# Performance work log

Measured on AMD Instinct MI355X. Metric: run time of the kernel, lower is better.

The kernel has to match this reference:

```python
import jax, jax.numpy as jnp
import numpy as np
import math

EPS_PHI = 1e-4
EPS_DEN = 1e-6

B, H, N, D = 4, 16, 4096, 64
M = 128  # num random features


def _phi(x, omega, is_query):
    # x: [B,H,N,D], omega: [M,D] -> [B,H,N,M]
    proj = jnp.einsum('bhnd,md->bhnm', x, omega)
    log_phi = proj - 0.5 * jnp.sum(x * x, axis=-1, keepdims=True)
    if is_query:
        log_phi = log_phi - jnp.max(log_phi, axis=-1, keepdims=True)
    else:
        log_phi = log_phi - jnp.max(log_phi)
    return jnp.exp(log_phi) / math.sqrt(omega.shape[0]) + EPS_PHI


def setup_inputs() -> dict:
    key = jax.random.key(0)
    kq, kk, kv, ko = jax.random.split(key, 4)
    return {
        'q': jax.random.normal(kq, (B, H, N, D), dtype=jnp.float32),
        'k': jax.random.normal(kk, (B, H, N, D), dtype=jnp.float32),
        'v': jax.random.normal(kv, (B, H, N, D), dtype=jnp.float32),
        'omega': jax.random.normal(ko, (M, D), dtype=jnp.float32),
    }


def reference(q, k, v, omega):
    scale = q.shape[-1] ** (-0.25)
    phi_q = _phi(q * scale, omega, is_query=True).astype(jnp.float32)
    phi_k = _phi(k * scale, omega, is_query=False).astype(jnp.float32)
    vf = v.astype(jnp.float32)

    b, h, n, m = phi_q.shape
    d = vf.shape[-1]
    # time-major for scan: [N,B,H,*]
    pq_t = jnp.moveaxis(phi_q, 2, 0)
    pk_t = jnp.moveaxis(phi_k, 2, 0)
    v_t = jnp.moveaxis(vf, 2, 0)

    S0 = jnp.zeros((b, h, m, d), jnp.float32)
    z0 = jnp.zeros((b, h, m), jnp.float32)

    def step(carry, inp):
        S, z = carry
        pq_i, pk_i, v_i = inp  # [B,H,M], [B,H,M], [B,H,D]
        S = S + jnp.einsum('bhm,bhd->bhmd', pk_i, v_i)
        z = z + pk_i
        num = jnp.einsum('bhm,bhmd->bhd', pq_i, S)
        den = jnp.sum(pq_i * z, axis=-1, keepdims=True) + EPS_DEN
        return (S, z), num / den

    _, out_t = jax.lax.scan(step, (S0, z0), (pq_t, pk_t, v_t))
    out = jnp.moveaxis(out_t, 0, 2)  # [B,H,N,D]
    return out.astype(q.dtype)
```

## Files before the change

kernel.cpp:

```cpp
#include <hip/hip_runtime.h>
#include <math.h>

#define Bq 4
#define Hq 16
#define Nq 4096
#define Dq 64
#define Mq 128
#define Cq 32
#define Lq 128
#define EPS_PHI 1e-4f
#define EPS_DEN 1e-6f
#define SCALE 0.35355339059327373f
#define INVSQRT_M 0.08838834764831845f
#define STATE_STRIDE 8320

#define KSTR 136

#define PERM(m) (((m) & 15) * 8 + ((m) >> 4))

typedef __attribute__((ext_vector_type(8))) short bf16x8;
typedef __attribute__((ext_vector_type(4))) short s16x4;
typedef __attribute__((ext_vector_type(4))) float f32x4;

static __device__ inline f32x4 mfma16(bf16x8 a, bf16x8 b, f32x4 c) {
    return __builtin_amdgcn_mfma_f32_16x16x32_bf16(a, b, c, 0, 0, 0);
}

static __device__ inline unsigned short f2bf(float f) {
    unsigned u = __builtin_bit_cast(unsigned, f);
    u += 0x7FFF + ((u >> 16) & 1);
    return (unsigned short)(u >> 16);
}

static __device__ inline bf16x8 gfrag(const float* p, float scale) {
    float4 a = *(const float4*)p;
    float4 b = *(const float4*)(p + 4);
    union { bf16x8 v; unsigned short s[8]; } u;
    u.s[0] = f2bf(a.x * scale); u.s[1] = f2bf(a.y * scale);
    u.s[2] = f2bf(a.z * scale); u.s[3] = f2bf(a.w * scale);
    u.s[4] = f2bf(b.x * scale); u.s[5] = f2bf(b.y * scale);
    u.s[6] = f2bf(b.z * scale); u.s[7] = f2bf(b.w * scale);
    return u.v;
}

static __device__ inline bf16x8 gfrag_h(const float* p, float* hs) {
    float4 a = *(const float4*)p;
    float4 b = *(const float4*)(p + 4);
    float x0 = a.x * SCALE, x1 = a.y * SCALE, x2 = a.z * SCALE, x3 = a.w * SCALE;
    float x4 = b.x * SCALE, x5 = b.y * SCALE, x6 = b.z * SCALE, x7 = b.w * SCALE;
    *hs += x0 * x0 + x1 * x1 + x2 * x2 + x3 * x3
         + x4 * x4 + x5 * x5 + x6 * x6 + x7 * x7;
    union { bf16x8 v; unsigned short s[8]; } u;
    u.s[0] = f2bf(x0); u.s[1] = f2bf(x1); u.s[2] = f2bf(x2); u.s[3] = f2bf(x3);
    u.s[4] = f2bf(x4); u.s[5] = f2bf(x5); u.s[6] = f2bf(x6); u.s[7] = f2bf(x7);
    return u.v;
}

static __device__ inline bf16x8 ones_frag() {
    union { bf16x8 v; unsigned short s[8]; } u;
    #pragma unroll
    for (int i = 0; i < 8; ++i) u.s[i] = 0x3F80;
    return u.v;
}

__global__ __launch_bounds__(256) void vconv_kernel(
    const float* __restrict__ vin, unsigned short* __restrict__ vT,
    float* __restrict__ csumV) {
    __shared__ __align__(16) unsigned short vt_lds[64 * KSTR];
    __shared__ float csum[4][64];
    const int t = threadIdx.x;
    const int bx = blockIdx.x;
    const int bh = bx >> 5;
    const int l0 = (bx & 31) * Lq;
    const float* vb = vin + ((size_t)bh * Nq + l0) * 64;
    const int d = t & 63, g = t >> 6;

    float s = 0.f;
    #pragma unroll
    for (int rep = 0; rep < 32; ++rep) {
        int l = rep * 4 + g;
        float x = vb[(size_t)l * 64 + d];
        s += x;
        vt_lds[d * KSTR + l] = f2bf(x);
    }
    csum[g][d] = s;
    __syncthreads();
    if (t < 64)
        csumV[(size_t)bx * 64 + t] = csum[0][t] + csum[1][t] + csum[2][t] + csum[3][t];
    unsigned short* vTb = vT + (size_t)bh * 64 * Nq + l0;
    #pragma unroll
    for (int rep = 0; rep < 4; ++rep) {
        int idx = rep * 256 + t;
        int dd = idx >> 4, seg = idx & 15;
        *(bf16x8*)&vTb[(size_t)dd * Nq + seg * 8] =
            *(const bf16x8*)&vt_lds[dd * KSTR + seg * 8];
    }
}

__global__ __launch_bounds__(256) void oconv_kernel(
    const float* __restrict__ omega, unsigned short* __restrict__ omb) {
    const int t = threadIdx.x;
    #pragma unroll
    for (int rep = 0; rep < 4; ++rep) {
        int g8 = rep * 256 + t;
        const float* p = omega + (size_t)g8 * 8;
        float4 a = *(const float4*)p;
        float4 b = *(const float4*)(p + 4);
        union { bf16x8 v; unsigned short s[8]; } u;
        u.s[0] = f2bf(a.x); u.s[1] = f2bf(a.y); u.s[2] = f2bf(a.z); u.s[3] = f2bf(a.w);
        u.s[4] = f2bf(b.x); u.s[5] = f2bf(b.y); u.s[6] = f2bf(b.z); u.s[7] = f2bf(b.w);
        *(bf16x8*)&omb[(size_t)g8 * 8] = u.v;
    }
}

__global__ __launch_bounds__(512, 4) void chunkstate_kernel(
    const float* __restrict__ kin, const unsigned short* __restrict__ omb,
    const unsigned short* __restrict__ vT,
    float* __restrict__ partial, float* __restrict__ Sbuf) {
    __shared__ __align__(16) unsigned short PKt[128 * KSTR];
    __shared__ float wred[8];
    const int t = threadIdx.x, w = t >> 6, lane = t & 63;
    const int c16 = lane & 15, qd = lane >> 4;
    const int bx = blockIdx.x;
    const int bh = bx >> 5;
    const int l0 = (bx & 31) * Lq;
    const size_t rowbase = (size_t)bh * Nq + l0;
    const float* kb = kin + rowbase * 64;

    f32x4 acc[8];
    float ssum = 0.f;
    #pragma unroll
    for (int nt = 0; nt < 8; ++nt) acc[nt] = (f32x4){0.f, 0.f, 0.f, 0.f};
    #pragma unroll
    for (int kt = 0; kt < 2; ++kt) {
        bf16x8 a = gfrag_h(kb + (size_t)(16 * w + c16) * 64 + kt * 32 + qd * 8, &ssum);
        #pragma unroll
        for (int nt = 0; nt < 8; ++nt) {
            bf16x8 b = *(const bf16x8*)&omb[(size_t)(16 * nt + c16) * 64 + kt * 32 + qd * 8];
            acc[nt] = mfma16(a, b, acc[nt]);
        }
    }
    ssum += __shfl_xor(ssum, 16);
    ssum += __shfl_xor(ssum, 32);
    const float h_red = 0.5f * ssum;
    const int row0 = 16 * w + 4 * qd;
    float h4[4];
    #pragma unroll
    for (int r = 0; r < 4; ++r) h4[r] = __shfl(h_red, 4 * qd + r);

    float lmax = -1e30f;
    #pragma unroll
    for (int r = 0; r < 4; ++r) {
        #pragma unroll
        for (int nt = 0; nt < 8; ++nt) lmax = fmaxf(lmax, acc[nt][r] - h4[r]);
    }
    #pragma unroll
    for (int o = 1; o <= 32; o <<= 1) lmax = fmaxf(lmax, __shfl_xor(lmax, o));
    if (lane == 0) wred[w] = lmax;
    __syncthreads();
    float mc = wred[0];
    #pragma unroll
    for (int i = 1; i < 8; ++i) mc = fmaxf(mc, wred[i]);
    if (t == 0) partial[bx] = mc;

    #pragma unroll
    for (int nt = 0; nt < 8; ++nt) {
        union { s16x4 v; unsigned short s[4]; } u;
        #pragma unroll
        for (int r = 0; r < 4; ++r) {
            float pk = __expf(acc[nt][r] - h4[r] - mc) * INVSQRT_M;
            u.s[r] = f2bf(pk);
        }
        *(s16x4*)&PKt[(16 * nt + c16) * KSTR + row0] = u.v;
    }
    __syncthreads();

    const unsigned short* vTb = vT + (size_t)bh * 64 * Nq + l0;
    f32x4 accS[4], accz;
    #pragma unroll
    for (int dt = 0; dt < 4; ++dt) accS[dt] = (f32x4){0.f, 0.f, 0.f, 0.f};
    accz = (f32x4){0.f, 0.f, 0.f, 0.f};
    const bf16x8 ones = ones_frag();
    #pragma unroll
    for (int kt = 0; kt < 4; ++kt) {
        bf16x8 bfr = *(const bf16x8*)&PKt[(16 * w + c16) * KSTR + kt * 32 + qd * 8];
        #pragma unroll
        for (int dt = 0; dt < 4; ++dt) {
            bf16x8 afr = *(const bf16x8*)&vTb[(size_t)(16 * dt + c16) * Nq + kt * 32 + qd * 8];
            accS[dt] = mfma16(afr, bfr, accS[dt]);
        }
        accz = mfma16(ones, bfr, accz);
    }
    float* sb = Sbuf + (size_t)bx * STATE_STRIDE;
    #pragma unroll
    for (int dt = 0; dt < 4; ++dt) {
        #pragma unroll
        for (int r = 0; r < 4; ++r)
            sb[(16 * dt + 4 * qd + r) * 128 + 16 * w + c16] = accS[dt][r];
    }
    if (qd == 0) sb[64 * 128 + 16 * w + c16] = accz[0];
}

__global__ void gmax_kernel(const float* __restrict__ partial, int n, float* __restrict__ gmax) {
    float m = -1e30f;
    for (int i = threadIdx.x; i < n; i += 256) m = fmaxf(m, partial[i]);
    #pragma unroll
    for (int o = 1; o <= 32; o <<= 1) m = fmaxf(m, __shfl_xor(m, o));
    __shared__ float w[4];
    if ((threadIdx.x & 63) == 0) w[threadIdx.x >> 6] = m;
    __syncthreads();
    if (threadIdx.x == 0) gmax[0] = fmaxf(fmaxf(w[0], w[1]), fmaxf(w[2], w[3]));
}

#define PBLK 33
__global__ __launch_bounds__(256) void prefix_kernel(
    const float* __restrict__ Sbuf, unsigned short* __restrict__ WtG,
    const float* __restrict__ csumV,
    const float* __restrict__ partial, const float* __restrict__ gmaxp) {
    const int bh = blockIdx.x / PBLK;
    const int e = (blockIdx.x % PBLK) * 256 + threadIdx.x;
    if (e >= STATE_STRIDE) return;
    const float gm = gmaxp[0];
    const int dz = e >> 7, m = e & 127;
    const int wcol = dz * 128 + PERM(m);
    const size_t base = (size_t)bh * Cq * STATE_STRIDE + e;

    float vals[Cq];
    #pragma unroll
    for (int c = 0; c < Cq; ++c) vals[c] = Sbuf[base + (size_t)c * STATE_STRIDE];

    float running = 0.f;
    #pragma unroll
    for (int c = 0; c < Cq; ++c) {
        const int cx = bh * Cq + c;
        float sc = __expf(partial[cx] - gm);
        float ep = (dz == 64) ? (EPS_PHI * 128.0f)
                              : (EPS_PHI * csumV[(size_t)cx * 64 + dz]);
        WtG[(size_t)cx * STATE_STRIDE + wcol] = f2bf(running);
        running += sc * vals[c] + ep;
    }
}

__global__ __launch_bounds__(512, 4) void replay_kernel(
    const float* __restrict__ q, const float* __restrict__ kin,
    const unsigned short* __restrict__ omb, const unsigned short* __restrict__ vT,
    const unsigned short* __restrict__ WtG,
    const float* __restrict__ gmaxp, float* __restrict__ out) {
    __shared__ __align__(16) unsigned short PK[128 * KSTR];
    const int t = threadIdx.x, w = t >> 6, lane = t & 63;
    const int c16 = lane & 15, qd = lane >> 4;
    const int bx = blockIdx.x;
    const int bh = bx >> 5;
    const int l0 = (bx & 31) * Lq;
    const size_t rowbase = (size_t)bh * Nq + l0;
    const float* qb = q + rowbase * 64;
    const float* kb = kin + rowbase * 64;
    const float gmax = gmaxp[0];
    const int row0 = 16 * w + 4 * qd;
    const int arow = 16 * w + c16;

    f32x4 accq[8], acck[8];
    float ssum = 0.f;
    #pragma unroll
    for (int nt = 0; nt < 8; ++nt) {
        accq[nt] = (f32x4){0.f, 0.f, 0.f, 0.f};
        acck[nt] = (f32x4){0.f, 0.f, 0.f, 0.f};
    }
    #pragma unroll
    for (int kt = 0; kt < 2; ++kt) {
        bf16x8 aq = gfrag(qb + (size_t)arow * 64 + kt * 32 + qd * 8, SCALE);
        bf16x8 ak = gfrag_h(kb + (size_t)arow * 64 + kt * 32 + qd * 8, &ssum);
        #pragma unroll
        for (int nt = 0; nt < 8; ++nt) {
            bf16x8 b = *(const bf16x8*)&omb[(size_t)(16 * nt + c16) * 64 + kt * 32 + qd * 8];
            accq[nt] = mfma16(aq, b, accq[nt]);
            acck[nt] = mfma16(ak, b, acck[nt]);
        }
    }
    ssum += __shfl_xor(ssum, 16);
    ssum += __shfl_xor(ssum, 32);
    const float h_red = 0.5f * ssum;

    unsigned pqu[4][4];
    #pragma unroll
    for (int r = 0; r < 4; ++r) {
        float mx = accq[0][r];
        #pragma unroll
        for (int nt = 1; nt < 8; ++nt) mx = fmaxf(mx, accq[nt][r]);
        mx = fmaxf(mx, __shfl_xor(mx, 1));
        mx = fmaxf(mx, __shfl_xor(mx, 2));
        mx = fmaxf(mx, __shfl_xor(mx, 4));
        mx = fmaxf(mx, __shfl_xor(mx, 8));
        #pragma unroll
        for (int i = 0; i < 4; ++i) {
            float lo = __expf(accq[2 * i][r]     - mx) * INVSQRT_M + EPS_PHI;
            float hi = __expf(accq[2 * i + 1][r] - mx) * INVSQRT_M + EPS_PHI;
            pqu[r][i] = (unsigned)f2bf(lo) | ((unsigned)f2bf(hi) << 16);
        }
    }
    bf16x8 bq[4];
    {
        const int rsel = c16 & 3;
        #pragma unroll
        for (int kt = 0; kt < 4; ++kt) {
            const int src = 4 * kt + qd + ((c16 >> 2) << 4);
            union { bf16x8 v; unsigned u[4]; } tt;
            #pragma unroll
            for (int i = 0; i < 4; ++i) {
                unsigned v0 = __shfl(pqu[0][i], src);
                unsigned v1 = __shfl(pqu[1][i], src);
                unsigned v2 = __shfl(pqu[2][i], src);
                unsigned v3 = __shfl(pqu[3][i], src);
                unsigned s01 = (rsel & 1) ? v1 : v0;
                unsigned s23 = (rsel & 1) ? v3 : v2;
                tt.u[i] = (rsel & 2) ? s23 : s01;
            }
            bq[kt] = tt.v;
        }
    }
    #pragma unroll
    for (int r = 0; r < 4; ++r) {
        float h = __shfl(h_red, 4 * qd + r);
        union { bf16x8 v; unsigned short s[8]; } u;
        #pragma unroll
        for (int nt = 0; nt < 8; ++nt)
            u.s[nt] = f2bf(__expf(acck[nt][r] - h - gmax) * INVSQRT_M + EPS_PHI);
        *(bf16x8*)&PK[(row0 + r) * KSTR + c16 * 8] = u.v;
    }
    __syncthreads();

    f32x4 a1[8];
    #pragma unroll
    for (int lt = 0; lt < 8; ++lt) {
        a1[lt] = (f32x4){0.f, 0.f, 0.f, 0.f};
        #pragma unroll
        for (int kt = 0; kt < 4; ++kt) {
            bf16x8 a = *(const bf16x8*)&PK[(16 * lt + c16) * KSTR + kt * 32 + qd * 8];
            a1[lt] = mfma16(a, bq[kt], a1[lt]);
        }
    }
    unsigned asu[8][2];
    #pragma unroll
    for (int lt = 0; lt < 8; ++lt) {
        const int lbase = 16 * lt + 4 * qd;
        float m0 = (lbase + 0 <= arow) ? a1[lt][0] : 0.f;
        float m1 = (lbase + 1 <= arow) ? a1[lt][1] : 0.f;
        float m2 = (lbase + 2 <= arow) ? a1[lt][2] : 0.f;
        float m3 = (lbase + 3 <= arow) ? a1[lt][3] : 0.f;
        asu[lt][0] = (unsigned)f2bf(m0) | ((unsigned)f2bf(m1) << 16);
        asu[lt][1] = (unsigned)f2bf(m2) | ((unsigned)f2bf(m3) << 16);
    }
    const unsigned short* vTb = vT + (size_t)bh * 64 * Nq + l0;
    const unsigned short* wg  = WtG + (size_t)bx * STATE_STRIDE;
    const bf16x8 ones = ones_frag();
    f32x4 acc2[5];
    #pragma unroll
    for (int nt = 0; nt < 5; ++nt) acc2[nt] = (f32x4){0.f, 0.f, 0.f, 0.f};
    {
        const int src0 = c16 + ((2 * qd) & 3) * 16;
        const int src1 = c16 + ((2 * qd + 1) & 3) * 16;
        const int hsel = qd >> 1;
        #pragma unroll
        for (int kt = 0; kt < 4; ++kt) {
            union { bf16x8 v; unsigned u[4]; } af;
            unsigned a00 = __shfl(asu[2 * kt][0], src0), a10 = __shfl(asu[2 * kt + 1][0], src0);
            unsigned a01 = __shfl(asu[2 * kt][1], src0), a11 = __shfl(asu[2 * kt + 1][1], src0);
            af.u[0] = hsel ? a10 : a00;
            af.u[1] = hsel ? a11 : a01;
            unsigned b00 = __shfl(asu[2 * kt][0], src1), b10 = __shfl(asu[2 * kt + 1][0], src1);
            unsigned b01 = __shfl(asu[2 * kt][1], src1), b11 = __shfl(asu[2 * kt + 1][1], src1);
            af.u[2] = hsel ? b10 : b00;
            af.u[3] = hsel ? b11 : b01;
            #pragma unroll
            for (int nt = 0; nt < 4; ++nt) {
                bf16x8 b = *(const bf16x8*)&vTb[(size_t)(16 * nt + c16) * Nq + kt * 32 + qd * 8];
                acc2[nt] = mfma16(af.v, b, acc2[nt]);
            }
            acc2[4] = mfma16(af.v, ones, acc2[4]);
        }
        #pragma unroll
        for (int kt = 0; kt < 4; ++kt) {
            #pragma unroll
            for (int nt = 0; nt < 4; ++nt) {
                bf16x8 b = *(const bf16x8*)&wg[(16 * nt + c16) * 128 + kt * 32 + qd * 8];
                acc2[nt] = mfma16(bq[kt], b, acc2[nt]);
            }
            bf16x8 bz = *(const bf16x8*)&wg[64 * 128 + kt * 32 + qd * 8];
            acc2[4] = mfma16(bq[kt], bz, acc2[4]);
        }
    }
    #pragma unroll
    for (int r = 0; r < 4; ++r) {
        float den = acc2[4][r] + EPS_DEN;
        float rd = 1.0f / den;
        #pragma unroll
        for (int nt = 0; nt < 4; ++nt)
            out[(rowbase + row0 + r) * 64 + 16 * nt + c16] = acc2[nt][r] * rd;
    }
}

extern "C" void kernel_launch(void* const* d_in, const int* in_sizes, int n_in,
                              void* d_out, int out_size, void* d_ws, size_t ws_size,
                              hipStream_t stream) {
    const float* q     = (const float*)d_in[0];
    const float* k     = (const float*)d_in[1];
    const float* v     = (const float*)d_in[2];
    const float* omega = (const float*)d_in[3];
    float* out = (float*)d_out;
    float* ws  = (float*)d_ws;

    const int nChunks = Bq * Hq * Cq;
    float* partial = ws;
    float* gmax    = partial + nChunks;
    float* csumV   = gmax + 16;
    unsigned short* omb = (unsigned short*)(csumV + (size_t)nChunks * 64);
    unsigned short* vT  = omb + 8192;
    unsigned short* WtG = vT + (size_t)64 * 64 * Nq;
    float* Sbuf = (float*)(WtG + (size_t)nChunks * STATE_STRIDE);

    vconv_kernel<<<nChunks, 256, 0, stream>>>(v, vT, csumV);
    oconv_kernel<<<1, 256, 0, stream>>>(omega, omb);
    chunkstate_kernel<<<nChunks, 512, 0, stream>>>(k, omb, vT, partial, Sbuf);
    gmax_kernel<<<1, 256, 0, stream>>>(partial, nChunks, gmax);
    prefix_kernel<<<64 * PBLK, 256, 0, stream>>>(Sbuf, WtG, csumV, partial, gmax);
    replay_kernel<<<nChunks, 512, 0, stream>>>(q, k, omb, vT, WtG, gmax, out);
}
```

Before: 416.6 us.

## Store omega, V and prefix state in MFMA fragment-major layout for coalesced loads

The producer kernels (oconv, vconv, prefix) now write the bf16 omega, the transposed V chunks and the prefix states in a fragment-major order. Each wave's MFMA B/A operand load then reads 64 consecutive 16-byte vectors instead of 16 strided rows. This removes uncoalesced, strided global reads in chunkstate and replay. The cost is more complex index math in the producers, and the prefix kernel's bf16 stores become scattered.

```diff
diff --git a/kernel.cpp b/kernel.cpp
--- a/kernel.cpp
+++ b/kernel.cpp
@@ -13,6 +13,8 @@
 #define SCALE 0.35355339059327373f
 #define INVSQRT_M 0.08838834764831845f
 #define STATE_STRIDE 8320
+#define VTF_STRIDE 8192
+#define WGF_STRIDE 8320
 
 #define KSTR 136
 
@@ -64,7 +66,7 @@
 }
 
 __global__ __launch_bounds__(256) void vconv_kernel(
-    const float* __restrict__ vin, unsigned short* __restrict__ vT,
+    const float* __restrict__ vin, unsigned short* __restrict__ vTf,
     float* __restrict__ csumV) {
     __shared__ __align__(16) unsigned short vt_lds[64 * KSTR];
     __shared__ float csum[4][64];
@@ -87,35 +89,38 @@
     __syncthreads();
     if (t < 64)
         csumV[(size_t)bx * 64 + t] = csum[0][t] + csum[1][t] + csum[2][t] + csum[3][t];
-    unsigned short* vTb = vT + (size_t)bh * 64 * Nq + l0;
+    unsigned short* dst = vTf + (size_t)bx * VTF_STRIDE;
     #pragma unroll
     for (int rep = 0; rep < 4; ++rep) {
         int idx = rep * 256 + t;
-        int dd = idx >> 4, seg = idx & 15;
-        *(bf16x8*)&vTb[(size_t)dd * Nq + seg * 8] =
-            *(const bf16x8*)&vt_lds[dd * KSTR + seg * 8];
+        int f = idx >> 6, lane = idx & 63;
+        int dt = f & 3, kt = f >> 2, c = lane & 15, qq = lane >> 4;
+        *(bf16x8*)&dst[(size_t)idx * 8] =
+            *(const bf16x8*)&vt_lds[(16 * dt + c) * KSTR + kt * 32 + qq * 8];
     }
 }
 
 __global__ __launch_bounds__(256) void oconv_kernel(
-    const float* __restrict__ omega, unsigned short* __restrict__ omb) {
+    const float* __restrict__ omega, unsigned short* __restrict__ ombF) {
     const int t = threadIdx.x;
     #pragma unroll
     for (int rep = 0; rep < 4; ++rep) {
         int g8 = rep * 256 + t;
-        const float* p = omega + (size_t)g8 * 8;
+        int m = g8 >> 3, d0 = (g8 & 7) * 8;
+        const float* p = omega + (size_t)m * 64 + d0;
         float4 a = *(const float4*)p;
         float4 b = *(const float4*)(p + 4);
         union { bf16x8 v; unsigned short s[8]; } u;
         u.s[0] = f2bf(a.x); u.s[1] = f2bf(a.y); u.s[2] = f2bf(a.z); u.s[3] = f2bf(a.w);
         u.s[4] = f2bf(b.x); u.s[5] = f2bf(b.y); u.s[6] = f2bf(b.z); u.s[7] = f2bf(b.w);
-        *(bf16x8*)&omb[(size_t)g8 * 8] = u.v;
+        int kt = d0 >> 5, qq = (d0 >> 3) & 3, nt = m >> 4, c = m & 15;
+        *(bf16x8*)&ombF[((size_t)(kt * 8 + nt) * 64 + qq * 16 + c) * 8] = u.v;
     }
 }
 
 __global__ __launch_bounds__(512, 4) void chunkstate_kernel(
-    const float* __restrict__ kin, const unsigned short* __restrict__ omb,
-    const unsigned short* __restrict__ vT,
+    const float* __restrict__ kin, const unsigned short* __restrict__ ombF,
+    const unsigned short* __restrict__ vTf,
     float* __restrict__ partial, float* __restrict__ Sbuf) {
     __shared__ __align__(16) unsigned short PKt[128 * KSTR];
     __shared__ float wred[8];
@@ -136,7 +141,7 @@
         bf16x8 a = gfrag_h(kb + (size_t)(16 * w + c16) * 64 + kt * 32 + qd * 8, &ssum);
         #pragma unroll
         for (int nt = 0; nt < 8; ++nt) {
-            bf16x8 b = *(const bf16x8*)&omb[(size_t)(16 * nt + c16) * 64 + kt * 32 + qd * 8];
+            bf16x8 b = *(const bf16x8*)&ombF[((size_t)(kt * 8 + nt) * 64 + lane) * 8];
             acc[nt] = mfma16(a, b, acc[nt]);
         }
     }
@@ -175,7 +180,7 @@
     }
     __syncthreads();
 
-    const unsigned short* vTb = vT + (size_t)bh * 64 * Nq + l0;
+    const unsigned short* vf = vTf + (size_t)bx * VTF_STRIDE;
     f32x4 accS[4], accz;
     #pragma unroll
     for (int dt = 0; dt < 4; ++dt) accS[dt] = (f32x4){0.f, 0.f, 0.f, 0.f};
@@ -186,7 +191,7 @@
         bf16x8 bfr = *(const bf16x8*)&PKt[(16 * w + c16) * KSTR + kt * 32 + qd * 8];
         #pragma unroll
         for (int dt = 0; dt < 4; ++dt) {
-            bf16x8 afr = *(const bf16x8*)&vTb[(size_t)(16 * dt + c16) * Nq + kt * 32 + qd * 8];
+            bf16x8 afr = *(const bf16x8*)&vf[((size_t)(kt * 4 + dt) * 64 + lane) * 8];
             accS[dt] = mfma16(afr, bfr, accS[dt]);
         }
         accz = mfma16(ones, bfr, accz);
@@ -214,7 +219,7 @@
 
 #define PBLK 33
 __global__ __launch_bounds__(256) void prefix_kernel(
-    const float* __restrict__ Sbuf, unsigned short* __restrict__ WtG,
+    const float* __restrict__ Sbuf, unsigned short* __restrict__ wgF,
     const float* __restrict__ csumV,
     const float* __restrict__ partial, const float* __restrict__ gmaxp) {
     const int bh = blockIdx.x / PBLK;
@@ -222,7 +227,15 @@
     if (e >= STATE_STRIDE) return;
     const float gm = gmaxp[0];
     const int dz = e >> 7, m = e & 127;
-    const int wcol = dz * 128 + PERM(m);
+    const int pm = PERM(m);
+    size_t widx;
+    if (dz == 64) {
+        widx = 8192 + pm;
+    } else {
+        const int f    = (pm >> 5) * 4 + (dz >> 4);
+        const int lane = ((pm >> 3) & 3) * 16 + (dz & 15);
+        widx = (size_t)f * 512 + lane * 8 + (pm & 7);
+    }
     const size_t base = (size_t)bh * Cq * STATE_STRIDE + e;
 
     float vals[Cq];
@@ -236,15 +249,15 @@
         float sc = __expf(partial[cx] - gm);
         float ep = (dz == 64) ? (EPS_PHI * 128.0f)
                               : (EPS_PHI * csumV[(size_t)cx * 64 + dz]);
-        WtG[(size_t)cx * STATE_STRIDE + wcol] = f2bf(running);
+        wgF[(size_t)cx * WGF_STRIDE + widx] = f2bf(running);
         running += sc * vals[c] + ep;
     }
 }
 
 __global__ __launch_bounds__(512, 4) void replay_kernel(
     const float* __restrict__ q, const float* __restrict__ kin,
-    const unsigned short* __restrict__ omb, const unsigned short* __restrict__ vT,
-    const unsigned short* __restrict__ WtG,
+    const unsigned short* __restrict__ ombF, const unsigned short* __restrict__ vTf,
+    const unsigned short* __restrict__ wgF,
     const float* __restrict__ gmaxp, float* __restrict__ out) {
     __shared__ __align__(16) unsigned short PK[128 * KSTR];
     const int t = threadIdx.x, w = t >> 6, lane = t & 63;
@@ -272,7 +285,7 @@
         bf16x8 ak = gfrag_h(kb + (size_t)arow * 64 + kt * 32 + qd * 8, &ssum);
         #pragma unroll
         for (int nt = 0; nt < 8; ++nt) {
-            bf16x8 b = *(const bf16x8*)&omb[(size_t)(16 * nt + c16) * 64 + kt * 32 + qd * 8];
+            bf16x8 b = *(const bf16x8*)&ombF[((size_t)(kt * 8 + nt) * 64 + lane) * 8];
             accq[nt] = mfma16(aq, b, accq[nt]);
             acck[nt] = mfma16(ak, b, acck[nt]);
         }
@@ -350,8 +363,8 @@
         asu[lt][0] = (unsigned)f2bf(m0) | ((unsigned)f2bf(m1) << 16);
         asu[lt][1] = (unsigned)f2bf(m2) | ((unsigned)f2bf(m3) << 16);
     }
-    const unsigned short* vTb = vT + (size_t)bh * 64 * Nq + l0;
-    const unsigned short* wg  = WtG + (size_t)bx * STATE_STRIDE;
+    const unsigned short* vf = vTf + (size_t)bx * VTF_STRIDE;
+    const unsigned short* wg = wgF + (size_t)bx * WGF_STRIDE;
     const bf16x8 ones = ones_frag();
     f32x4 acc2[5];
     #pragma unroll
@@ -373,7 +386,7 @@
             af.u[3] = hsel ? b11 : b01;
             #pragma unroll
             for (int nt = 0; nt < 4; ++nt) {
-                bf16x8 b = *(const bf16x8*)&vTb[(size_t)(16 * nt + c16) * Nq + kt * 32 + qd * 8];
+                bf16x8 b = *(const bf16x8*)&vf[((size_t)(kt * 4 + nt) * 64 + lane) * 8];
                 acc2[nt] = mfma16(af.v, b, acc2[nt]);
             }
             acc2[4] = mfma16(af.v, ones, acc2[4]);
@@ -382,10 +395,10 @@
         for (int kt = 0; kt < 4; ++kt) {
             #pragma unroll
             for (int nt = 0; nt < 4; ++nt) {
-                bf16x8 b = *(const bf16x8*)&wg[(16 * nt + c16) * 128 + kt * 32 + qd * 8];
+                bf16x8 b = *(const bf16x8*)&wg[((size_t)(kt * 4 + nt) * 64 + lane) * 8];
                 acc2[nt] = mfma16(bq[kt], b, acc2[nt]);
             }
-            bf16x8 bz = *(const bf16x8*)&wg[64 * 128 + kt * 32 + qd * 8];
+            bf16x8 bz = *(const bf16x8*)&wg[8192 + kt * 32 + qd * 8];
             acc2[4] = mfma16(bq[kt], bz, acc2[4]);
         }
     }
@@ -413,15 +426,15 @@
     float* partial = ws;
     float* gmax    = partial + nChunks;
     float* csumV   = gmax + 16;
-    unsigned short* omb = (unsigned short*)(csumV + (size_t)nChunks * 64);
-    unsigned short* vT  = omb + 8192;
-    unsigned short* WtG = vT + (size_t)64 * 64 * Nq;
-    float* Sbuf = (float*)(WtG + (size_t)nChunks * STATE_STRIDE);
-
-    vconv_kernel<<<nChunks, 256, 0, stream>>>(v, vT, csumV);
-    oconv_kernel<<<1, 256, 0, stream>>>(omega, omb);
-    chunkstate_kernel<<<nChunks, 512, 0, stream>>>(k, omb, vT, partial, Sbuf);
+    unsigned short* ombF = (unsigned short*)(csumV + (size_t)nChunks * 64);
+    unsigned short* vTf  = ombF + 8192;
+    unsigned short* wgF  = vTf + (size_t)nChunks * VTF_STRIDE;
+    float* Sbuf = (float*)(wgF + (size_t)nChunks * WGF_STRIDE);
+
+    vconv_kernel<<<nChunks, 256, 0, stream>>>(v, vTf, csumV);
+    oconv_kernel<<<1, 256, 0, stream>>>(omega, ombF);
+    chunkstate_kernel<<<nChunks, 512, 0, stream>>>(k, ombF, vTf, partial, Sbuf);
     gmax_kernel<<<1, 256, 0, stream>>>(partial, nChunks, gmax);
-    prefix_kernel<<<64 * PBLK, 256, 0, stream>>>(Sbuf, WtG, csumV, partial, gmax);
-    replay_kernel<<<nChunks, 512, 0, stream>>>(q, k, omb, vT, WtG, gmax, out);
-}
+    prefix_kernel<<<64 * PBLK, 256, 0, stream>>>(Sbuf, wgF, csumV, partial, gmax);
+    replay_kernel<<<nChunks, 512, 0, stream>>>(q, k, ombF, vTf, wgF, gmax, out);
+}
```

New measurement: 350.3 us. 1.19x faster.
